# Kernel optimization log

Measured on AMD Instinct MI355X. Metric: run time of the kernel, lower is better.

## Reference

```python
import jax, jax.numpy as jnp
import numpy as np

N_NODES = 65536
N_EDGES = 1048576
D_FEAT = 64
K_HOPS = 10
ALPHA = 0.1


def setup_inputs() -> dict:
    key = jax.random.key(0)
    k1, k2 = jax.random.split(key, 2)
    x = jax.random.normal(k1, (N_NODES, D_FEAT), dtype=jnp.float32)
    edge_index = jax.random.randint(k2, (2, N_EDGES), 0, N_NODES, dtype=jnp.int32)
    # PPR init of the learnable polynomial coefficients (length K+1)
    temp = ALPHA * (1.0 - ALPHA) ** np.arange(K_HOPS + 1)
    temp[-1] = (1.0 - ALPHA) ** K_HOPS
    temp = jnp.asarray(temp, dtype=jnp.float32)
    return {"x": x, "temp": temp, "edge_index": edge_index}


def reference(x, temp, edge_index):
    # GCN-normalized adjacency with self-loops (gcn_norm, homophily=True path):
    #   A_hat = D^{-1/2} (A + I) D^{-1/2}
    N = x.shape[0]
    K = temp.shape[0] - 1
    loops = jnp.arange(N, dtype=edge_index.dtype)
    src = jnp.concatenate([edge_index[0], loops])  # message sources (x_j)
    dst = jnp.concatenate([edge_index[1], loops])  # aggregation targets
    ones = jnp.ones(src.shape[0], dtype=x.dtype)
    deg = jax.ops.segment_sum(ones, dst, num_segments=N)  # self-loops => deg > 0
    dinv = jax.lax.rsqrt(deg)
    norm = dinv[src] * dinv[dst]  # [E+N]

    # hidden = temp[K-1]*x; then K-1 propagation hops accumulating temp[k]*A_hat^m x
    hidden = temp[K - 1] * x
    h = x
    for k in range(K - 2, -1, -1):
        # sparse propagate: scatter-add of norm-weighted gathered source features
        h = jax.ops.segment_sum(norm[:, None] * h[src], dst, num_segments=N)
        hidden = hidden + temp[k] * h
    return hidden
```

## Files before the change

kernel.cpp:

```cpp
#include <hip/hip_runtime.h>
#include <hip/hip_fp16.h>

#define N_NODES 65536
#define N_EDGES 1048576
#define BUCKET  64

typedef float vfloat4 __attribute__((ext_vector_type(4)));
typedef unsigned long long ull;


__global__ void count_deg(const int* __restrict__ dst, int* __restrict__ counts,
                          int* __restrict__ rank) {
    int e = blockIdx.x * blockDim.x + threadIdx.x;
    if (e < N_EDGES) rank[e] = atomicAdd(&counts[dst[e]], 1);
}

__global__ void compute_dinv(const int* __restrict__ counts, float* __restrict__ dinv) {
    int v = blockIdx.x * blockDim.x + threadIdx.x;
    if (v < N_NODES) dinv[v] = rsqrtf((float)(counts[v] + 1));
}

__global__ void scatter_src(const int* __restrict__ src, const int* __restrict__ dst,
                            const int* __restrict__ rank,
                            unsigned short* __restrict__ csr) {
    int e = blockIdx.x * blockDim.x + threadIdx.x;
    if (e >= N_EDGES) return;
    csr[dst[e] * BUCKET + rank[e]] = (unsigned short)src[e];
}

__global__ void cvt_x(const float* __restrict__ x, const float* __restrict__ dinv,
                      __half* __restrict__ t0, __half* __restrict__ xh) {
    int i = blockIdx.x * blockDim.x + threadIdx.x;
    int v = i >> 4;
    float dv = dinv[v];
    float4 val = ((const float4*)x)[i];
    __half2 xl = __floats2half2_rn(val.x, val.y);
    __half2 xh2 = __floats2half2_rn(val.z, val.w);
    ull ox = ((ull)(*(const unsigned*)&xh2) << 32) | (*(const unsigned*)&xl);
    __half2 tl = __floats2half2_rn(dv * val.x, dv * val.y);
    __half2 th = __floats2half2_rn(dv * val.z, dv * val.w);
    ull ot = ((ull)(*(const unsigned*)&th) << 32) | (*(const unsigned*)&tl);
    ((ull*)xh)[i] = ox;
    ((ull*)t0)[i] = ot;
}

__global__ void __launch_bounds__(256) hop_kernel(
        const __half* __restrict__ tab, const __half* __restrict__ xh,
        __half* __restrict__ tab_out, float* __restrict__ out_f32,
        const float* __restrict__ temp, const int* __restrict__ counts,
        const unsigned short* __restrict__ csr, const float* __restrict__ dinv,
        int k) {
    int gtid = blockIdx.x * blockDim.x + threadIdx.x;
    int wave = __builtin_amdgcn_readfirstlane(gtid >> 6);
    int lane = gtid & 63;
    int q = lane >> 4;
    int f = lane & 15;

    int v0 = wave * 4;
    float tk = temp[k];
    float sc = (k == 1) ? temp[0] : 1.0f;

    int4 cv = *(const int4*)(counts + v0);
    int cnt[4] = {cv.x, cv.y, cv.z, cv.w};
    float4 dvv = *(const float4*)(dinv + v0);
    float dv[4] = {dvv.x, dvv.y, dvv.z, dvv.w};

    int maxc = max(max(cnt[0], cnt[1]), max(cnt[2], cnt[3]));
    int iters = (maxc + 15) >> 4;

    const ull* t2 = (const ull*)tab;
    float a0[4] = {0.f, 0.f, 0.f, 0.f};
    float a1[4] = {0.f, 0.f, 0.f, 0.f};
    float a2[4] = {0.f, 0.f, 0.f, 0.f};
    float a3[4] = {0.f, 0.f, 0.f, 0.f};

    for (int r = 0; r < iters; ++r) {
        int e0 = r * 16;
        #pragma unroll
        for (int j = 0; j < 4; ++j) {
            const int4* bp = (const int4*)(csr + (v0 + j) * BUCKET + e0);
            int4 sgA = bp[0];
            int4 sgB = bp[1];
            #pragma unroll
            for (int g = 0; g < 4; ++g) {
                int4 sg = (g & 2) ? sgB : sgA;
                int word = (g & 1) ? ((q & 2) ? sg.w : sg.z)
                                   : ((q & 2) ? sg.y : sg.x);
                int s = (word >> ((q & 1) * 16)) & 0xffff;
                ull row = t2[s * 16 + f];
                row = ((e0 + 4 * g + q) < cnt[j]) ? row : 0ull;
                unsigned rl = (unsigned)row, rh = (unsigned)(row >> 32);
                float2 lo = __half22float2(*(const __half2*)&rl);
                float2 hi = __half22float2(*(const __half2*)&rh);
                a0[j] += lo.x; a1[j] += lo.y; a2[j] += hi.x; a3[j] += hi.y;
            }
        }
    }

    #pragma unroll
    for (int j = 0; j < 4; ++j) {
        a0[j] += __shfl_xor(a0[j], 16); a0[j] += __shfl_xor(a0[j], 32);
        a1[j] += __shfl_xor(a1[j], 16); a1[j] += __shfl_xor(a1[j], 32);
        a2[j] += __shfl_xor(a2[j], 16); a2[j] += __shfl_xor(a2[j], 32);
        a3[j] += __shfl_xor(a3[j], 16); a3[j] += __shfl_xor(a3[j], 32);
    }

    #pragma unroll
    for (int j = 0; j < 4; ++j) {
        int v = v0 + j;
        ull sx = ((const ull*)xh)[v * 16 + f];
        ull st = t2[v * 16 + f];
        unsigned sxl = (unsigned)sx, sxh2 = (unsigned)(sx >> 32);
        unsigned stl = (unsigned)st, sth = (unsigned)(st >> 32);
        float2 xlo = __half22float2(*(const __half2*)&sxl);
        float2 xhi = __half22float2(*(const __half2*)&sxh2);
        float2 slo = __half22float2(*(const __half2*)&stl);
        float2 shi = __half22float2(*(const __half2*)&sth);
        float m = sc * dv[j];
        float r0 = m * (a0[j] + slo.x) + tk * xlo.x;
        float r1 = m * (a1[j] + slo.y) + tk * xlo.y;
        float r2 = m * (a2[j] + shi.x) + tk * xhi.x;
        float r3 = m * (a3[j] + shi.y) + tk * xhi.y;
        if (q == 0) {
            if (k == 9) {
                vfloat4 o = {r0, r1, r2, r3};
                ((vfloat4*)out_f32)[v * 16 + f] = o;
            } else {
                float d2 = dv[j];
                __half2 plo = __floats2half2_rn(d2 * r0, d2 * r1);
                __half2 phi = __floats2half2_rn(d2 * r2, d2 * r3);
                ull o = ((ull)(*(const unsigned*)&phi) << 32)
                      | (*(const unsigned*)&plo);
                ((ull*)tab_out)[v * 16 + f] = o;
            }
        }
    }
}

extern "C" void kernel_launch(void* const* d_in, const int* in_sizes, int n_in,
                              void* d_out, int out_size, void* d_ws, size_t ws_size,
                              hipStream_t stream) {
    const float* x    = (const float*)d_in[0];
    const float* temp = (const float*)d_in[1];
    const int*   ei   = (const int*)d_in[2];
    const int* src = ei;
    const int* dst = ei + N_EDGES;
    float* out = (float*)d_out;

    char* ws = (char*)d_ws;
    int*            counts = (int*)            (ws + 0x000000);
    float*          dinv   = (float*)          (ws + 0x040000);
    int*            rank   = (int*)            (ws + 0x080000);
    unsigned short* csr    = (unsigned short*) (ws + 0x480000);
    __half*         xh     = (__half*)         (ws + 0xC80000);
    __half*         tA     = (__half*)         (ws + 0x1480000);
    __half*         tB     = (__half*)         (ws + 0x1C80000);

    (void)hipMemsetAsync(counts, 0, N_NODES * sizeof(int), stream);
    (void)hipMemsetAsync(csr, 0, N_NODES * BUCKET * sizeof(unsigned short), stream);

    count_deg<<<N_EDGES / 256, 256, 0, stream>>>(dst, counts, rank);
    compute_dinv<<<N_NODES / 256, 256, 0, stream>>>(counts, dinv);
    scatter_src<<<N_EDGES / 256, 256, 0, stream>>>(src, dst, rank, csr);
    cvt_x<<<(N_NODES * 16) / 256, 256, 0, stream>>>(x, dinv, tA, xh);

    const int hop_blocks = (N_NODES / 4) * 64 / 256;
    const __half* gin = tA;
    for (int k = 1; k <= 9; ++k) {
        __half* gout = (k & 1) ? tB : tA;
        hop_kernel<<<hop_blocks, 256, 0, stream>>>(gin, xh, gout, out, temp,
                                                   counts, csr, dinv, k);
        gin = gout;
    }
}
```

Measured before the change: 362.4 us.

## Fuse CSR build into one kernel and widen hop gathers to 16-byte rows

Merges the degree-count and CSR scatter kernels into one pass, which drops the rank array and one launch. The hop kernel now has each lane gather 16 bytes (8 halves) per neighbour row instead of 8, so a wave handles 8 neighbours per step. Per-node iteration also skips sub-chunks past that node's degree. In exchange each lane holds twice as many accumulators and does three shuffle rounds instead of two, which raises register pressure.

```diff
diff --git a/kernel.cpp b/kernel.cpp
--- a/kernel.cpp
+++ b/kernel.cpp
@@ -9,23 +9,18 @@
 typedef unsigned long long ull;
 
 
-__global__ void count_deg(const int* __restrict__ dst, int* __restrict__ counts,
-                          int* __restrict__ rank) {
+__global__ void build_csr(const int* __restrict__ src, const int* __restrict__ dst,
+                          int* __restrict__ counts, unsigned short* __restrict__ csr) {
     int e = blockIdx.x * blockDim.x + threadIdx.x;
-    if (e < N_EDGES) rank[e] = atomicAdd(&counts[dst[e]], 1);
+    if (e >= N_EDGES) return;
+    int d = dst[e];
+    int r = atomicAdd(&counts[d], 1);
+    if (r < BUCKET) csr[d * BUCKET + r] = (unsigned short)src[e];
 }
 
 __global__ void compute_dinv(const int* __restrict__ counts, float* __restrict__ dinv) {
     int v = blockIdx.x * blockDim.x + threadIdx.x;
     if (v < N_NODES) dinv[v] = rsqrtf((float)(counts[v] + 1));
-}
-
-__global__ void scatter_src(const int* __restrict__ src, const int* __restrict__ dst,
-                            const int* __restrict__ rank,
-                            unsigned short* __restrict__ csr) {
-    int e = blockIdx.x * blockDim.x + threadIdx.x;
-    if (e >= N_EDGES) return;
-    csr[dst[e] * BUCKET + rank[e]] = (unsigned short)src[e];
 }
 
 __global__ void cvt_x(const float* __restrict__ x, const float* __restrict__ dinv,
@@ -53,85 +48,105 @@
     int gtid = blockIdx.x * blockDim.x + threadIdx.x;
     int wave = __builtin_amdgcn_readfirstlane(gtid >> 6);
     int lane = gtid & 63;
-    int q = lane >> 4;
-    int f = lane & 15;
+    int q = lane >> 3;
+    int f = lane & 7;
 
     int v0 = wave * 4;
     float tk = temp[k];
     float sc = (k == 1) ? temp[0] : 1.0f;
 
     int4 cv = *(const int4*)(counts + v0);
-    int cnt[4] = {cv.x, cv.y, cv.z, cv.w};
+    int cnt[4];
+    cnt[0] = min(cv.x, BUCKET); cnt[1] = min(cv.y, BUCKET);
+    cnt[2] = min(cv.z, BUCKET); cnt[3] = min(cv.w, BUCKET);
     float4 dvv = *(const float4*)(dinv + v0);
     float dv[4] = {dvv.x, dvv.y, dvv.z, dvv.w};
 
     int maxc = max(max(cnt[0], cnt[1]), max(cnt[2], cnt[3]));
-    int iters = (maxc + 15) >> 4;
+    int iters = (maxc + 7) >> 3;
 
-    const ull* t2 = (const ull*)tab;
-    float a0[4] = {0.f, 0.f, 0.f, 0.f};
-    float a1[4] = {0.f, 0.f, 0.f, 0.f};
-    float a2[4] = {0.f, 0.f, 0.f, 0.f};
-    float a3[4] = {0.f, 0.f, 0.f, 0.f};
+    const uint4* t4 = (const uint4*)tab;
+    float a[4][8] = {};
 
-    for (int r = 0; r < iters; ++r) {
-        int e0 = r * 16;
+    for (int r = 0; r < iters; r += 2) {
         #pragma unroll
         for (int j = 0; j < 4; ++j) {
-            const int4* bp = (const int4*)(csr + (v0 + j) * BUCKET + e0);
-            int4 sgA = bp[0];
-            int4 sgB = bp[1];
             #pragma unroll
-            for (int g = 0; g < 4; ++g) {
-                int4 sg = (g & 2) ? sgB : sgA;
-                int word = (g & 1) ? ((q & 2) ? sg.w : sg.z)
+            for (int gg = 0; gg < 2; ++gg) {
+                int e0 = (r + gg) * 8;
+                if (e0 >= cnt[j]) continue;
+                int4 sg = *(const int4*)(csr + (v0 + j) * BUCKET + e0);
+                int word = (q & 4) ? ((q & 2) ? sg.w : sg.z)
                                    : ((q & 2) ? sg.y : sg.x);
                 int s = (word >> ((q & 1) * 16)) & 0xffff;
-                ull row = t2[s * 16 + f];
-                row = ((e0 + 4 * g + q) < cnt[j]) ? row : 0ull;
-                unsigned rl = (unsigned)row, rh = (unsigned)(row >> 32);
-                float2 lo = __half22float2(*(const __half2*)&rl);
-                float2 hi = __half22float2(*(const __half2*)&rh);
-                a0[j] += lo.x; a1[j] += lo.y; a2[j] += hi.x; a3[j] += hi.y;
+                uint4 row = t4[s * 8 + f];
+                bool valid = (e0 + q) < cnt[j];
+                unsigned rx = valid ? row.x : 0u;
+                unsigned ry = valid ? row.y : 0u;
+                unsigned rz = valid ? row.z : 0u;
+                unsigned rw = valid ? row.w : 0u;
+                float2 p0 = __half22float2(*(const __half2*)&rx);
+                float2 p1 = __half22float2(*(const __half2*)&ry);
+                float2 p2 = __half22float2(*(const __half2*)&rz);
+                float2 p3 = __half22float2(*(const __half2*)&rw);
+                a[j][0] += p0.x; a[j][1] += p0.y;
+                a[j][2] += p1.x; a[j][3] += p1.y;
+                a[j][4] += p2.x; a[j][5] += p2.y;
+                a[j][6] += p3.x; a[j][7] += p3.y;
             }
         }
     }
 
     #pragma unroll
     for (int j = 0; j < 4; ++j) {
-        a0[j] += __shfl_xor(a0[j], 16); a0[j] += __shfl_xor(a0[j], 32);
-        a1[j] += __shfl_xor(a1[j], 16); a1[j] += __shfl_xor(a1[j], 32);
-        a2[j] += __shfl_xor(a2[j], 16); a2[j] += __shfl_xor(a2[j], 32);
-        a3[j] += __shfl_xor(a3[j], 16); a3[j] += __shfl_xor(a3[j], 32);
+        #pragma unroll
+        for (int t = 0; t < 8; ++t) {
+            a[j][t] += __shfl_xor(a[j][t], 8);
+            a[j][t] += __shfl_xor(a[j][t], 16);
+            a[j][t] += __shfl_xor(a[j][t], 32);
+        }
     }
 
     #pragma unroll
     for (int j = 0; j < 4; ++j) {
         int v = v0 + j;
-        ull sx = ((const ull*)xh)[v * 16 + f];
-        ull st = t2[v * 16 + f];
-        unsigned sxl = (unsigned)sx, sxh2 = (unsigned)(sx >> 32);
-        unsigned stl = (unsigned)st, sth = (unsigned)(st >> 32);
-        float2 xlo = __half22float2(*(const __half2*)&sxl);
-        float2 xhi = __half22float2(*(const __half2*)&sxh2);
-        float2 slo = __half22float2(*(const __half2*)&stl);
-        float2 shi = __half22float2(*(const __half2*)&sth);
+        uint4 sx = ((const uint4*)xh)[v * 8 + f];
+        uint4 st = t4[v * 8 + f];
+        float2 x0 = __half22float2(*(const __half2*)&sx.x);
+        float2 x1 = __half22float2(*(const __half2*)&sx.y);
+        float2 x2 = __half22float2(*(const __half2*)&sx.z);
+        float2 x3 = __half22float2(*(const __half2*)&sx.w);
+        float2 s0 = __half22float2(*(const __half2*)&st.x);
+        float2 s1 = __half22float2(*(const __half2*)&st.y);
+        float2 s2 = __half22float2(*(const __half2*)&st.z);
+        float2 s3 = __half22float2(*(const __half2*)&st.w);
         float m = sc * dv[j];
-        float r0 = m * (a0[j] + slo.x) + tk * xlo.x;
-        float r1 = m * (a1[j] + slo.y) + tk * xlo.y;
-        float r2 = m * (a2[j] + shi.x) + tk * xhi.x;
-        float r3 = m * (a3[j] + shi.y) + tk * xhi.y;
+        float r0 = m * (a[j][0] + s0.x) + tk * x0.x;
+        float r1 = m * (a[j][1] + s0.y) + tk * x0.y;
+        float r2 = m * (a[j][2] + s1.x) + tk * x1.x;
+        float r3 = m * (a[j][3] + s1.y) + tk * x1.y;
+        float r4 = m * (a[j][4] + s2.x) + tk * x2.x;
+        float r5 = m * (a[j][5] + s2.y) + tk * x2.y;
+        float r6 = m * (a[j][6] + s3.x) + tk * x3.x;
+        float r7 = m * (a[j][7] + s3.y) + tk * x3.y;
         if (q == 0) {
             if (k == 9) {
-                vfloat4 o = {r0, r1, r2, r3};
-                ((vfloat4*)out_f32)[v * 16 + f] = o;
+                vfloat4 o0 = {r0, r1, r2, r3};
+                vfloat4 o1 = {r4, r5, r6, r7};
+                ((vfloat4*)out_f32)[v * 16 + 2 * f]     = o0;
+                ((vfloat4*)out_f32)[v * 16 + 2 * f + 1] = o1;
             } else {
                 float d2 = dv[j];
-                __half2 plo = __floats2half2_rn(d2 * r0, d2 * r1);
-                __half2 phi = __floats2half2_rn(d2 * r2, d2 * r3);
-                ull o = ((ull)(*(const unsigned*)&phi) << 32)
-                      | (*(const unsigned*)&plo);
-                ((ull*)tab_out)[v * 16 + f] = o;
+                __half2 h0 = __floats2half2_rn(d2 * r0, d2 * r1);
+                __half2 h1 = __floats2half2_rn(d2 * r2, d2 * r3);
+                __half2 h2 = __floats2half2_rn(d2 * r4, d2 * r5);
+                __half2 h3 = __floats2half2_rn(d2 * r6, d2 * r7);
+                uint4 o;
+                o.x = *(const unsigned*)&h0;
+                o.y = *(const unsigned*)&h1;
+                o.z = *(const unsigned*)&h2;
+                o.w = *(const unsigned*)&h3;
+                ((uint4*)tab_out)[v * 8 + f] = o;
             }
         }
     }
@@ -150,7 +165,6 @@
     char* ws = (char*)d_ws;
     int*            counts = (int*)            (ws + 0x000000);
     float*          dinv   = (float*)          (ws + 0x040000);
-    int*            rank   = (int*)            (ws + 0x080000);
     unsigned short* csr    = (unsigned short*) (ws + 0x480000);
     __half*         xh     = (__half*)         (ws + 0xC80000);
     __half*         tA     = (__half*)         (ws + 0x1480000);
@@ -159,9 +173,8 @@
     (void)hipMemsetAsync(counts, 0, N_NODES * sizeof(int), stream);
     (void)hipMemsetAsync(csr, 0, N_NODES * BUCKET * sizeof(unsigned short), stream);
 
-    count_deg<<<N_EDGES / 256, 256, 0, stream>>>(dst, counts, rank);
+    build_csr<<<N_EDGES / 256, 256, 0, stream>>>(src, dst, counts, csr);
     compute_dinv<<<N_NODES / 256, 256, 0, stream>>>(counts, dinv);
-    scatter_src<<<N_EDGES / 256, 256, 0, stream>>>(src, dst, rank, csr);
     cvt_x<<<(N_NODES * 16) / 256, 256, 0, stream>>>(x, dinv, tA, xh);
 
     const int hop_blocks = (N_NODES / 4) * 64 / 256;
```

New measurement: 467.6 us. 29.1% more time.

## Assign one wavefront per node and drop per-edge bounds masking in hop kernel

Applied to the files above, without the earlier changes.

The hop kernel now gives each wavefront a single destination node instead of four, so its loop count follows that node's own degree rather than the maximum of four. The per-edge validity select is removed. Padded CSR slots, which are zero and so gather row 0, are accounted for by subtracting (padded count × row 0) after the reduction. Bucket overflow is now clamped at 64 in both scatter and count. The change launches four times as many waves, each with less work, and relies on padding slots holding zeros. Gathered fp16 rows and the subtraction can add small rounding error.

```diff
diff --git a/kernel.cpp b/kernel.cpp
--- a/kernel.cpp
+++ b/kernel.cpp
@@ -25,7 +25,8 @@
                             unsigned short* __restrict__ csr) {
     int e = blockIdx.x * blockDim.x + threadIdx.x;
     if (e >= N_EDGES) return;
-    csr[dst[e] * BUCKET + rank[e]] = (unsigned short)src[e];
+    int r = rank[e];
+    if (r < BUCKET) csr[dst[e] * BUCKET + r] = (unsigned short)src[e];
 }
 
 __global__ void cvt_x(const float* __restrict__ x, const float* __restrict__ dinv,
@@ -51,88 +52,76 @@
         const unsigned short* __restrict__ csr, const float* __restrict__ dinv,
         int k) {
     int gtid = blockIdx.x * blockDim.x + threadIdx.x;
-    int wave = __builtin_amdgcn_readfirstlane(gtid >> 6);
+    int v = __builtin_amdgcn_readfirstlane(gtid >> 6);
     int lane = gtid & 63;
     int q = lane >> 4;
     int f = lane & 15;
 
-    int v0 = wave * 4;
     float tk = temp[k];
     float sc = (k == 1) ? temp[0] : 1.0f;
 
-    int4 cv = *(const int4*)(counts + v0);
-    int cnt[4] = {cv.x, cv.y, cv.z, cv.w};
-    float4 dvv = *(const float4*)(dinv + v0);
-    float dv[4] = {dvv.x, dvv.y, dvv.z, dvv.w};
-
-    int maxc = max(max(cnt[0], cnt[1]), max(cnt[2], cnt[3]));
-    int iters = (maxc + 15) >> 4;
+    int cnt = min(counts[v], BUCKET);
+    float dv = dinv[v];
+    int iters = (cnt + 15) >> 4;
 
     const ull* t2 = (const ull*)tab;
-    float a0[4] = {0.f, 0.f, 0.f, 0.f};
-    float a1[4] = {0.f, 0.f, 0.f, 0.f};
-    float a2[4] = {0.f, 0.f, 0.f, 0.f};
-    float a3[4] = {0.f, 0.f, 0.f, 0.f};
+    float a0 = 0.f, a1 = 0.f, a2 = 0.f, a3 = 0.f;
 
     for (int r = 0; r < iters; ++r) {
         int e0 = r * 16;
+        const int4* bp = (const int4*)(csr + v * BUCKET + e0);
+        int4 sgA = bp[0];
+        int4 sgB = bp[1];
         #pragma unroll
-        for (int j = 0; j < 4; ++j) {
-            const int4* bp = (const int4*)(csr + (v0 + j) * BUCKET + e0);
-            int4 sgA = bp[0];
-            int4 sgB = bp[1];
-            #pragma unroll
-            for (int g = 0; g < 4; ++g) {
-                int4 sg = (g & 2) ? sgB : sgA;
-                int word = (g & 1) ? ((q & 2) ? sg.w : sg.z)
-                                   : ((q & 2) ? sg.y : sg.x);
-                int s = (word >> ((q & 1) * 16)) & 0xffff;
-                ull row = t2[s * 16 + f];
-                row = ((e0 + 4 * g + q) < cnt[j]) ? row : 0ull;
-                unsigned rl = (unsigned)row, rh = (unsigned)(row >> 32);
-                float2 lo = __half22float2(*(const __half2*)&rl);
-                float2 hi = __half22float2(*(const __half2*)&rh);
-                a0[j] += lo.x; a1[j] += lo.y; a2[j] += hi.x; a3[j] += hi.y;
-            }
+        for (int g = 0; g < 4; ++g) {
+            int4 sg = (g & 2) ? sgB : sgA;
+            int word = (g & 1) ? ((q & 2) ? sg.w : sg.z)
+                               : ((q & 2) ? sg.y : sg.x);
+            int s = (word >> ((q & 1) * 16)) & 0xffff;
+            ull row = t2[s * 16 + f];
+            unsigned rl = (unsigned)row, rh = (unsigned)(row >> 32);
+            float2 lo = __half22float2(*(const __half2*)&rl);
+            float2 hi = __half22float2(*(const __half2*)&rh);
+            a0 += lo.x; a1 += lo.y; a2 += hi.x; a3 += hi.y;
         }
     }
 
-    #pragma unroll
-    for (int j = 0; j < 4; ++j) {
-        a0[j] += __shfl_xor(a0[j], 16); a0[j] += __shfl_xor(a0[j], 32);
-        a1[j] += __shfl_xor(a1[j], 16); a1[j] += __shfl_xor(a1[j], 32);
-        a2[j] += __shfl_xor(a2[j], 16); a2[j] += __shfl_xor(a2[j], 32);
-        a3[j] += __shfl_xor(a3[j], 16); a3[j] += __shfl_xor(a3[j], 32);
-    }
+    a0 += __shfl_xor(a0, 16); a0 += __shfl_xor(a0, 32);
+    a1 += __shfl_xor(a1, 16); a1 += __shfl_xor(a1, 32);
+    a2 += __shfl_xor(a2, 16); a2 += __shfl_xor(a2, 32);
+    a3 += __shfl_xor(a3, 16); a3 += __shfl_xor(a3, 32);
 
-    #pragma unroll
-    for (int j = 0; j < 4; ++j) {
-        int v = v0 + j;
-        ull sx = ((const ull*)xh)[v * 16 + f];
-        ull st = t2[v * 16 + f];
-        unsigned sxl = (unsigned)sx, sxh2 = (unsigned)(sx >> 32);
-        unsigned stl = (unsigned)st, sth = (unsigned)(st >> 32);
-        float2 xlo = __half22float2(*(const __half2*)&sxl);
-        float2 xhi = __half22float2(*(const __half2*)&sxh2);
-        float2 slo = __half22float2(*(const __half2*)&stl);
-        float2 shi = __half22float2(*(const __half2*)&sth);
-        float m = sc * dv[j];
-        float r0 = m * (a0[j] + slo.x) + tk * xlo.x;
-        float r1 = m * (a1[j] + slo.y) + tk * xlo.y;
-        float r2 = m * (a2[j] + shi.x) + tk * xhi.x;
-        float r3 = m * (a3[j] + shi.y) + tk * xhi.y;
-        if (q == 0) {
-            if (k == 9) {
-                vfloat4 o = {r0, r1, r2, r3};
-                ((vfloat4*)out_f32)[v * 16 + f] = o;
-            } else {
-                float d2 = dv[j];
-                __half2 plo = __floats2half2_rn(d2 * r0, d2 * r1);
-                __half2 phi = __floats2half2_rn(d2 * r2, d2 * r3);
-                ull o = ((ull)(*(const unsigned*)&phi) << 32)
-                      | (*(const unsigned*)&plo);
-                ((ull*)tab_out)[v * 16 + f] = o;
-            }
+    float nh = (float)(iters * 16 - cnt);
+    ull z = t2[f];
+    unsigned zl = (unsigned)z, zh = (unsigned)(z >> 32);
+    float2 zlo = __half22float2(*(const __half2*)&zl);
+    float2 zhi = __half22float2(*(const __half2*)&zh);
+    a0 -= nh * zlo.x; a1 -= nh * zlo.y; a2 -= nh * zhi.x; a3 -= nh * zhi.y;
+
+    ull sx = ((const ull*)xh)[v * 16 + f];
+    ull st = t2[v * 16 + f];
+    unsigned sxl = (unsigned)sx, sxh2 = (unsigned)(sx >> 32);
+    unsigned stl = (unsigned)st, sth = (unsigned)(st >> 32);
+    float2 xlo = __half22float2(*(const __half2*)&sxl);
+    float2 xhi = __half22float2(*(const __half2*)&sxh2);
+    float2 slo = __half22float2(*(const __half2*)&stl);
+    float2 shi = __half22float2(*(const __half2*)&sth);
+    float m = sc * dv;
+    float r0 = m * (a0 + slo.x) + tk * xlo.x;
+    float r1 = m * (a1 + slo.y) + tk * xlo.y;
+    float r2 = m * (a2 + shi.x) + tk * xhi.x;
+    float r3 = m * (a3 + shi.y) + tk * xhi.y;
+    if (q == 0) {
+        if (k == 9) {
+            vfloat4 o = {r0, r1, r2, r3};
+            ((vfloat4*)out_f32)[v * 16 + f] = o;
+        } else {
+            float d2 = dv;
+            __half2 plo = __floats2half2_rn(d2 * r0, d2 * r1);
+            __half2 phi = __floats2half2_rn(d2 * r2, d2 * r3);
+            ull o = ((ull)(*(const unsigned*)&phi) << 32)
+                  | (*(const unsigned*)&plo);
+            ((ull*)tab_out)[v * 16 + f] = o;
         }
     }
 }
@@ -164,7 +153,7 @@
     scatter_src<<<N_EDGES / 256, 256, 0, stream>>>(src, dst, rank, csr);
     cvt_x<<<(N_NODES * 16) / 256, 256, 0, stream>>>(x, dinv, tA, xh);
 
-    const int hop_blocks = (N_NODES / 4) * 64 / 256;
+    const int hop_blocks = N_NODES * 64 / 256;
     const __half* gin = tA;
     for (int k = 1; k <= 9; ++k) {
         __half* gout = (k & 1) ? tB : tA;
```

New measurement: 379.6 us. +4.8%, slower.
